# Kernel tuning notes

Hardware: AMD Instinct MI355X
Metric: run time of the kernel (lower is better)

## Reference

```python
import jax, jax.numpy as jnp
import numpy as np

B, L, H, NH = 4, 512, 512, 8
DK = H // NH
REPR_IN, REPR_HID = 53, 32
EPS = 1e-5


def setup_inputs() -> dict:
    key = jax.random.key(0)
    ks = jax.random.split(key, 12)
    x = jax.random.normal(ks[0], (B, L, H), dtype=jnp.float32)
    mask = jax.random.randint(ks[1], (B, L), 0, 2, dtype=jnp.int32)
    refCov = jax.random.normal(ks[2], (B, L, L, REPR_IN), dtype=jnp.float32)
    def lin(k, fan_in, fan_out):
        return jax.random.normal(k, (fan_in, fan_out), dtype=jnp.float32) / np.sqrt(fan_in)
    Wv = lin(ks[3], H, H); bv = jnp.zeros((H,), jnp.float32)
    W1 = lin(ks[4], REPR_IN, REPR_HID); b1 = jnp.zeros((REPR_HID,), jnp.float32)
    W2 = lin(ks[5], REPR_HID, NH); b2 = jnp.zeros((NH,), jnp.float32)
    Wo = lin(ks[6], H, H); bo = jnp.zeros((H,), jnp.float32)
    gamma = jnp.ones((H,), jnp.float32); beta = jnp.zeros((H,), jnp.float32)
    return {"x": x, "mask": mask, "refCov": refCov, "Wv": Wv, "bv": bv,
            "W1": W1, "b1": b1, "W2": W2, "b2": b2, "Wo": Wo, "bo": bo,
            "gamma": gamma, "beta": beta}


def reference(x, mask, refCov, Wv, bv, W1, b1, W2, b2, Wo, bo, gamma, beta):
    Bx, Lx, Hx = x.shape
    residual = x
    # value projection -> (B, NH, L, DK)
    value = (x @ Wv + bv).reshape(Bx, Lx, NH, DK).transpose(0, 2, 1, 3)
    # per-pair MLP on refCov: (B, L, L, 53) -> (B, L, L, NH)
    h1 = jax.nn.relu(refCov @ W1 + b1)
    scores = jnp.transpose(h1 @ W2 + b2, (0, 3, 1, 2))  # (B, NH, L, L)
    # pairwise mask and softmax
    m = mask.astype(bool)
    mask2d = m[:, :, None] & m[:, None, :]              # (B, L, L)
    masked = jnp.where(mask2d[:, None, :, :], scores, -jnp.inf)
    all_inf_rows = ~jnp.any(mask2d, axis=-1)            # (B, L) rows fully masked
    masked = jnp.where(all_inf_rows[:, None, :, None], 0.0, masked)
    attn = jax.nn.softmax(masked, axis=-1)
    # weighted sum and output projection
    out = jnp.einsum('bhij,bhjd->bhid', attn, value)
    out = out.transpose(0, 2, 1, 3).reshape(Bx, Lx, Hx)
    out = out @ Wo + bo
    # residual + LayerNorm
    y = residual + out
    mu = jnp.mean(y, axis=-1, keepdims=True)
    var = jnp.var(y, axis=-1, keepdims=True)
    return (y - mu) / jnp.sqrt(var + EPS) * gamma + beta
```

## Files before the change

kernel.cpp:

```cpp
#include <hip/hip_runtime.h>
#include <hip/hip_bf16.h>
#include <math.h>

#define B 4
#define L 512
#define H 512
#define NH 8
#define DK 64
#define RIN 53
#define RHID 32

using short8 = __attribute__((ext_vector_type(8))) short;
using ushort8v = __attribute__((ext_vector_type(8))) unsigned short;
using f32x4 = __attribute__((ext_vector_type(4))) float;

__device__ __forceinline__ float waveReduceSum(float v) {
#pragma unroll
  for (int off = 32; off > 0; off >>= 1) v += __shfl_xor(v, off, 64);
  return v;
}

__device__ __forceinline__ unsigned short cvt_bf16(float f) {
  __hip_bfloat16 h = __float2bfloat16(f);
  return __builtin_bit_cast(unsigned short, h);
}

__global__ __launch_bounds__(512) void prep_kernel(
    const int* __restrict__ mask, int* __restrict__ jidx, int* __restrict__ nv,
    const float* __restrict__ Wv, const float* __restrict__ Wo,
    unsigned short* __restrict__ WvT, unsigned short* __restrict__ WoT) {
  const int bid = blockIdx.x;
  const int tid = threadIdx.x;
  if (bid < 4) {
    const int b = bid;
    const int lane = tid & 63, wv = tid >> 6;
    __shared__ int wtot[8], woff[8];
    const int m = (mask[b * 512 + tid] != 0);
    const unsigned long long bal = __ballot(m);
    const int lpre = __popcll(bal & ((1ull << lane) - 1ull));
    if (lane == 0) wtot[wv] = __popcll(bal);
    __syncthreads();
    if (tid == 0) {
      int acc = 0;
#pragma unroll
      for (int q = 0; q < 8; ++q) {
        woff[q] = acc;
        acc += wtot[q];
      }
      nv[b] = acc;
    }
    __syncthreads();
    if (m) jidx[b * 512 + woff[wv] + lpre] = tid;
    return;
  }
  const int t = bid - 4;
  const int matsel = t >> 6;
  const int tile = t & 63;
  const float* W = matsel ? Wo : Wv;
  unsigned short* WT = matsel ? WoT : WvT;
  const int k0 = (tile & 7) * 64, n0 = (tile >> 3) * 64;
  __shared__ float sT[64][65];
  {
    const int r = tid >> 3, c0 = (tid & 7) * 8;
    const float4 v0 = *(const float4*)(W + (size_t)(k0 + r) * 512 + n0 + c0);
    const float4 v1 = *(const float4*)(W + (size_t)(k0 + r) * 512 + n0 + c0 + 4);
    sT[r][c0] = v0.x; sT[r][c0 + 1] = v0.y; sT[r][c0 + 2] = v0.z; sT[r][c0 + 3] = v0.w;
    sT[r][c0 + 4] = v1.x; sT[r][c0 + 5] = v1.y; sT[r][c0 + 6] = v1.z; sT[r][c0 + 7] = v1.w;
  }
  __syncthreads();
  {
    const int n = tid >> 3, c0 = (tid & 7) * 8;
    ushort8v o;
#pragma unroll
    for (int cc = 0; cc < 8; ++cc) o[cc] = cvt_bf16(sT[c0 + cc][n]);
    *(ushort8v*)(WT + (size_t)(n0 + n) * 512 + k0 + c0) = o;
  }
}

#define GEMM_SMEM 13824
template <int AMODE, int OMODE>
__device__ __forceinline__ void gemm32x64(
    char* __restrict__ smem, const void* __restrict__ Aq, int lda,
    const unsigned short* __restrict__ Bs, int ldb,
    const float* __restrict__ bias, void* __restrict__ Cp, int ldc) {
  unsigned short* sA = (unsigned short*)smem;
  unsigned short* sB = (unsigned short*)(smem + 4608);
  float(*sC)[68] = (float(*)[68])smem;
  const int tid = threadIdx.x;
  const int w = tid >> 6, l = tid & 63, g = l >> 4, a = l & 15;
  const int wm = (w >> 1) * 16, wn = (w & 1) * 32;
  f32x4 acc0 = {}, acc1 = {};
  const int ar = tid >> 3, ak = (tid & 7) * 8;

  auto loadA = [&](int k0) {
    ushort8v r;
    if constexpr (AMODE == 1) {
      const float* Af = (const float*)Aq;
      const float* p = Af + (size_t)ar * lda + k0 + ak;
      const float4 v0 = *(const float4*)p;
      const float4 v1 = *(const float4*)(p + 4);
      r[0] = cvt_bf16(v0.x); r[1] = cvt_bf16(v0.y);
      r[2] = cvt_bf16(v0.z); r[3] = cvt_bf16(v0.w);
      r[4] = cvt_bf16(v1.x); r[5] = cvt_bf16(v1.y);
      r[6] = cvt_bf16(v1.z); r[7] = cvt_bf16(v1.w);
    } else {
      const unsigned short* Ab = (const unsigned short*)Aq;
      r = *(const ushort8v*)(Ab + (size_t)ar * lda + k0 + ak);
    }
    return r;
  };
  auto loadB = [&](int k0, int q) {
    const int s = tid + q * 256;
    return *(const ushort8v*)(Bs + (size_t)(s >> 3) * ldb + k0 + (s & 7) * 8);
  };

  ushort8v aR = loadA(0);
  ushort8v bR0 = loadB(0, 0), bR1 = loadB(0, 1);
  for (int k0 = 0; k0 < 512; k0 += 64) {
    *(ushort8v*)(&sA[ar * 72 + ak]) = aR;
    *(ushort8v*)(&sB[ar * 72 + ak]) = bR0;
    *(ushort8v*)(&sB[(ar + 32) * 72 + ak]) = bR1;
    __syncthreads();
    if (k0 < 448) {
      aR = loadA(k0 + 64);
      bR0 = loadB(k0 + 64, 0);
      bR1 = loadB(k0 + 64, 1);
    }
#pragma unroll
    for (int ks = 0; ks < 2; ++ks) {
      const short8 af = *(const short8*)(&sA[(wm + a) * 72 + ks * 32 + g * 8]);
      const short8 bf0 = *(const short8*)(&sB[(wn + a) * 72 + ks * 32 + g * 8]);
      const short8 bf1 =
          *(const short8*)(&sB[(wn + 16 + a) * 72 + ks * 32 + g * 8]);
      acc0 = __builtin_amdgcn_mfma_f32_16x16x32_bf16(af, bf0, acc0, 0, 0, 0);
      acc1 = __builtin_amdgcn_mfma_f32_16x16x32_bf16(af, bf1, acc1, 0, 0, 0);
    }
    __syncthreads();
  }

#pragma unroll
  for (int r = 0; r < 4; ++r) {
    sC[wm + g * 4 + r][wn + a] = acc0[r];
    sC[wm + g * 4 + r][wn + 16 + a] = acc1[r];
  }
  __syncthreads();

  if constexpr (OMODE == 2) {
    const int n = tid >> 2, iq = (tid & 3) * 8;
    const float bv = bias ? bias[n] : 0.f;
    ushort8v o;
#pragma unroll
    for (int cc = 0; cc < 8; ++cc) o[cc] = cvt_bf16(sC[iq + cc][n] + bv);
    *(ushort8v*)((unsigned short*)Cp + (size_t)n * ldc + iq) = o;
  } else {
    const int m = tid >> 3, c8 = (tid & 7) * 8;
    float v[8];
#pragma unroll
    for (int cc = 0; cc < 8; ++cc) {
      v[cc] = sC[m][c8 + cc];
      if (bias) v[cc] += bias[c8 + cc];
    }
    if constexpr (OMODE == 1) {
      ushort8v o;
#pragma unroll
      for (int cc = 0; cc < 8; ++cc) o[cc] = cvt_bf16(v[cc]);
      *(ushort8v*)((unsigned short*)Cp + (size_t)m * ldc + c8) = o;
    } else {
      *(float4*)((float*)Cp + (size_t)m * ldc + c8) =
          make_float4(v[0], v[1], v[2], v[3]);
      *(float4*)((float*)Cp + (size_t)m * ldc + c8 + 4) =
          make_float4(v[4], v[5], v[6], v[7]);
    }
  }
}

#define FUSED_SMEM 15616
__global__ __launch_bounds__(256) void fused_scores_value_kernel(
    const float* __restrict__ refCov, const int* __restrict__ mask,
    const int* __restrict__ jidx, const int* __restrict__ nvArr,
    const float* __restrict__ W1, const float* __restrict__ b1,
    const float* __restrict__ W2, const float* __restrict__ b2,
    unsigned short* __restrict__ attnb, const float* __restrict__ x,
    const unsigned short* __restrict__ WvT, const float* __restrict__ bv,
    unsigned short* __restrict__ valT) {
  __shared__ __align__(16) char smem[FUSED_SMEM];
  const int tid = threadIdx.x;

  if (blockIdx.x >= 2048) {
    const int gb = blockIdx.x - 2048;
    const int n0 = (gb & 7) * 64;
    const int m0 = (gb >> 3) * 32;
    const int b = m0 >> 9, i0 = m0 & 511;
    gemm32x64<1, 2>(smem, x + (size_t)m0 * 512, 512, WvT + (size_t)n0 * 512,
                    512, bv + n0,
                    valT + (size_t)b * 262144 + (size_t)n0 * 512 + i0, 512);
    return;
  }

  unsigned short* sH1 = (unsigned short*)smem;
  int* sJ = (int*)(smem + 5120);
  unsigned short* sOut = (unsigned short*)(smem + 7168);
  float(*redbuf)[16] = (float(*)[16])(smem + 15360);

  const int b = blockIdx.x >> 9;
  const int i = blockIdx.x & (L - 1);
  const int w = tid >> 6;
  const int l = tid & 63;
  const int g = l >> 4;
  const int a = l & 15;

  const int mi = mask[b * L + i];
  const int nv = nvArr[b];

  if (mi == 0 || nv == 0) {
    const ushort4 u4 = {0x3B00u, 0x3B00u, 0x3B00u, 0x3B00u};
#pragma unroll
    for (int q = 0; q < 4; ++q) {
      const int f4 = q * 256 + tid;
      const int h = f4 >> 7;
      const int c4 = f4 & 127;
      *(ushort4*)(attnb + ((size_t)(b * NH + h) * L + i) * L + c4 * 4) = u4;
    }
    return;
  }

  sJ[tid] = jidx[b * 512 + tid];
  sJ[tid + 256] = jidx[b * 512 + 256 + tid];

  short8 w1f[2][2];
#pragma unroll
  for (int ks = 0; ks < 2; ++ks)
#pragma unroll
    for (int nt = 0; nt < 2; ++nt)
#pragma unroll
      for (int e = 0; e < 8; ++e) {
        const int k = ks * 32 + g * 8 + e;
        w1f[ks][nt][e] =
            (k < RIN) ? (short)cvt_bf16(W1[k * RHID + nt * 16 + a]) : (short)0;
      }
  short8 w2f;
#pragma unroll
  for (int e = 0; e < 8; ++e) {
    const int k = g * 8 + e;
    w2f[e] = (a < NH) ? (short)cvt_bf16(W2[k * NH + a]) : (short)0;
  }
  const float b1v0 = b1[a];
  const float b1v1 = b1[16 + a];
  const float b2v = (a < NH) ? b2[a] : 0.f;

  __syncthreads();

  const int NT = (nv + 15) >> 4;
  f32x4 sc[8];

#pragma unroll
  for (int mt = 0; mt < 8; ++mt) {
    const int t = mt * 4 + w;
    if (t >= NT) continue;
    const int s = t * 16 + a;
    const int j = sJ[(s < nv) ? s : (nv - 1)];
    const float* rp = refCov + ((size_t)((b << 9) + i) * 512 + j) * RIN;

    const float4 u0 = *(const float4*)(rp + g * 8);
    const float4 u1 = *(const float4*)(rp + g * 8 + 4);
    const int base0 = (g < 3) ? (32 + g * 8) : 32;
    const int base1 = (g == 0) ? 36 : (g == 1) ? 44 : 49;
    const float4 v0 = *(const float4*)(rp + base0);
    const float4 v1 = *(const float4*)(rp + base1);
    float t1[8];
    if (g < 3) {
      t1[0] = v0.x; t1[1] = v0.y; t1[2] = v0.z; t1[3] = v0.w;
    } else {
      t1[0] = 0.f; t1[1] = 0.f; t1[2] = 0.f; t1[3] = 0.f;
    }
    if (g < 2) {
      t1[4] = v1.x; t1[5] = v1.y; t1[6] = v1.z; t1[7] = v1.w;
    } else if (g == 2) {
      t1[4] = v1.w;
      t1[5] = 0.f; t1[6] = 0.f; t1[7] = 0.f;
    } else {
      t1[4] = 0.f; t1[5] = 0.f; t1[6] = 0.f; t1[7] = 0.f;
    }
    short8 af0, af1;
    af0[0] = (short)cvt_bf16(u0.x); af0[1] = (short)cvt_bf16(u0.y);
    af0[2] = (short)cvt_bf16(u0.z); af0[3] = (short)cvt_bf16(u0.w);
    af0[4] = (short)cvt_bf16(u1.x); af0[5] = (short)cvt_bf16(u1.y);
    af0[6] = (short)cvt_bf16(u1.z); af0[7] = (short)cvt_bf16(u1.w);
#pragma unroll
    for (int e = 0; e < 8; ++e) af1[e] = (short)cvt_bf16(t1[e]);

    f32x4 h0 = f32x4{b1v0, b1v0, b1v0, b1v0};
    f32x4 h1v = f32x4{b1v1, b1v1, b1v1, b1v1};
    h0 = __builtin_amdgcn_mfma_f32_16x16x32_bf16(af0, w1f[0][0], h0, 0, 0, 0);
    h1v = __builtin_amdgcn_mfma_f32_16x16x32_bf16(af0, w1f[0][1], h1v, 0, 0, 0);
    h0 = __builtin_amdgcn_mfma_f32_16x16x32_bf16(af1, w1f[1][0], h0, 0, 0, 0);
    h1v = __builtin_amdgcn_mfma_f32_16x16x32_bf16(af1, w1f[1][1], h1v, 0, 0, 0);

#pragma unroll
    for (int r = 0; r < 4; ++r) {
      sH1[(w * 16 + g * 4 + r) * 40 + a] = cvt_bf16(fmaxf(h0[r], 0.f));
      sH1[(w * 16 + g * 4 + r) * 40 + 16 + a] = cvt_bf16(fmaxf(h1v[r], 0.f));
    }

    const short8 af2 = *(const short8*)(&sH1[(w * 16 + a) * 40 + g * 8]);
    f32x4 acc = f32x4{b2v, b2v, b2v, b2v};
    sc[mt] = __builtin_amdgcn_mfma_f32_16x16x32_bf16(af2, w2f, acc, 0, 0, 0);
  }

  float mx = -INFINITY;
#pragma unroll
  for (int mt = 0; mt < 8; ++mt) {
    const int t = mt * 4 + w;
    if (t >= NT) continue;
#pragma unroll
    for (int r = 0; r < 4; ++r) {
      const int s = t * 16 + g * 4 + r;
      if (s < nv) mx = fmaxf(mx, sc[mt][r]);
    }
  }
  mx = fmaxf(mx, __shfl_xor(mx, 16, 64));
  mx = fmaxf(mx, __shfl_xor(mx, 32, 64));
  if (g == 0) redbuf[w][a] = mx;
  __syncthreads();
  const float rmax = fmaxf(fmaxf(redbuf[0][a], redbuf[1][a]),
                           fmaxf(redbuf[2][a], redbuf[3][a]));
  __syncthreads();

  float lsum = 0.f;
#pragma unroll
  for (int mt = 0; mt < 8; ++mt) {
    const int t = mt * 4 + w;
    if (t >= NT) continue;
#pragma unroll
    for (int r = 0; r < 4; ++r) {
      const int s = t * 16 + g * 4 + r;
      const float e = (s < nv) ? __expf(sc[mt][r] - rmax) : 0.f;
      sc[mt][r] = e;
      lsum += e;
    }
  }
  lsum += __shfl_xor(lsum, 16, 64);
  lsum += __shfl_xor(lsum, 32, 64);
  if (g == 0) redbuf[w][a] = lsum;
  __syncthreads();
  const float rsum = redbuf[0][a] + redbuf[1][a] + redbuf[2][a] + redbuf[3][a];
  const float inv = 1.f / rsum;

  {
    const ushort8v z{};
    *(ushort8v*)(&sOut[tid * 16]) = z;
    *(ushort8v*)(&sOut[tid * 16 + 8]) = z;
  }
  __syncthreads();
  if (a < NH) {
#pragma unroll
    for (int mt = 0; mt < 8; ++mt) {
      const int t = mt * 4 + w;
      if (t >= NT) continue;
#pragma unroll
      for (int r = 0; r < 4; ++r) {
        const int s = t * 16 + g * 4 + r;
        if (s < nv) sOut[a * 512 + sJ[s]] = cvt_bf16(sc[mt][r] * inv);
      }
    }
  }
  __syncthreads();
  {
    const int h = tid >> 5, off = (tid & 31) * 16;
    unsigned short* dst = attnb + ((size_t)(b * NH + h) * L + i) * L + off;
    *(ushort8v*)dst = *(const ushort8v*)(&sOut[h * 512 + off]);
    *(ushort8v*)(dst + 8) = *(const ushort8v*)(&sOut[h * 512 + off + 8]);
  }
}

__global__ __launch_bounds__(256) void attn_value_kernel(
    const unsigned short* __restrict__ attnb,
    const unsigned short* __restrict__ valT, unsigned short* __restrict__ ctx) {
  __shared__ __align__(16) char smem[GEMM_SMEM];
  const int bid = blockIdx.x;
  const int it = bid & 15, h = (bid >> 4) & 7, b = bid >> 7;
  const int i0 = it * 32;
  gemm32x64<0, 1>(smem, attnb + ((size_t)((b * 8 + h) * 512 + i0)) * 512, 512,
                  valT + (size_t)b * 262144 + (size_t)(h * 64) * 512, 512,
                  nullptr, ctx + ((size_t)(b * 512 + i0)) * 512 + h * 64, 512);
}

__global__ __launch_bounds__(256) void gemm_proj_kernel(
    const unsigned short* __restrict__ ctx,
    const unsigned short* __restrict__ WoT, const float* __restrict__ bo,
    float* __restrict__ proj) {
  __shared__ __align__(16) char smem[GEMM_SMEM];
  const int n0 = blockIdx.x * 64;
  const int m0 = blockIdx.y * 32;
  gemm32x64<0, 0>(smem, ctx + (size_t)m0 * 512, 512, WoT + (size_t)n0 * 512,
                  512, bo + n0, proj + (size_t)m0 * 512 + n0, 512);
}

__global__ __launch_bounds__(256) void residual_ln_kernel(
    const float* __restrict__ x, const float* __restrict__ proj,
    const float* __restrict__ gamma, const float* __restrict__ beta,
    float* __restrict__ out) {
  const int row = blockIdx.x;
  const int tid = threadIdx.x;
  __shared__ float redS[4], redQ[4];
  float y[2];
  float ls = 0.f, lq = 0.f;
#pragma unroll
  for (int p = 0; p < 2; ++p) {
    const int c = tid + p * 256;
    const float v = x[(size_t)row * H + c] + proj[(size_t)row * H + c];
    y[p] = v;
    ls += v;
    lq += v * v;
  }
  const int lane = tid & 63, wave = tid >> 6;
  ls = waveReduceSum(ls);
  lq = waveReduceSum(lq);
  if (lane == 0) {
    redS[wave] = ls;
    redQ[wave] = lq;
  }
  __syncthreads();
  const float sum = redS[0] + redS[1] + redS[2] + redS[3];
  const float sq = redQ[0] + redQ[1] + redQ[2] + redQ[3];
  const float mu = sum * (1.f / H);
  const float var = sq * (1.f / H) - mu * mu;
  const float inv = rsqrtf(var + 1e-5f);
#pragma unroll
  for (int p = 0; p < 2; ++p) {
    const int c = tid + p * 256;
    out[(size_t)row * H + c] = (y[p] - mu) * inv * gamma[c] + beta[c];
  }
}

extern "C" void kernel_launch(void* const* d_in, const int* in_sizes, int n_in,
                              void* d_out, int out_size, void* d_ws,
                              size_t ws_size, hipStream_t stream) {
  const float* x = (const float*)d_in[0];
  const int* mask = (const int*)d_in[1];
  const float* refCov = (const float*)d_in[2];
  const float* Wv = (const float*)d_in[3];
  const float* bv = (const float*)d_in[4];
  const float* W1 = (const float*)d_in[5];
  const float* b1 = (const float*)d_in[6];
  const float* W2 = (const float*)d_in[7];
  const float* b2 = (const float*)d_in[8];
  const float* Wo = (const float*)d_in[9];
  const float* bo = (const float*)d_in[10];
  const float* gamma = (const float*)d_in[11];
  const float* beta = (const float*)d_in[12];
  float* out = (float*)d_out;

  const size_t n_attn = (size_t)B * NH * L * L;
  const size_t n_blh = (size_t)B * L * H;
  const size_t n_w = (size_t)H * H;
  unsigned short* attnb = (unsigned short*)d_ws;
  unsigned short* valT = attnb + n_attn;
  unsigned short* ctx = valT + n_blh;
  unsigned short* WvT = ctx + n_blh;
  unsigned short* WoT = WvT + n_w;
  float* proj = (float*)(WoT + n_w);
  int* jidx = (int*)(proj + n_blh);
  int* nv = jidx + B * L;
  const size_t needed =
      (n_attn + 2 * n_blh + 2 * n_w) * 2 + n_blh * 4 + (B * L + B) * 4;
  if (ws_size < needed) return;

  const int M = B * L;

  prep_kernel<<<132, 512, 0, stream>>>(mask, jidx, nv, Wv, Wo, WvT, WoT);
  fused_scores_value_kernel<<<2048 + 512, 256, 0, stream>>>(
      refCov, mask, jidx, nv, W1, b1, W2, b2, attnb, x, WvT, bv, valT);
  attn_value_kernel<<<512, 256, 0, stream>>>(attnb, valT, ctx);
  gemm_proj_kernel<<<dim3(8, M / 32), 256, 0, stream>>>(ctx, WoT, bo, proj);
  residual_ln_kernel<<<M, 256, 0, stream>>>(x, proj, gamma, beta, out);
}
```

Before: 61.06 us.

## Fuse output projection GEMM with residual add and LayerNorm

```diff
diff --git a/kernel.cpp b/kernel.cpp
--- a/kernel.cpp
+++ b/kernel.cpp
@@ -13,12 +13,6 @@
 using short8 = __attribute__((ext_vector_type(8))) short;
 using ushort8v = __attribute__((ext_vector_type(8))) unsigned short;
 using f32x4 = __attribute__((ext_vector_type(4))) float;
-
-__device__ __forceinline__ float waveReduceSum(float v) {
-#pragma unroll
-  for (int off = 32; off > 0; off >>= 1) v += __shfl_xor(v, off, 64);
-  return v;
-}
 
 __device__ __forceinline__ unsigned short cvt_bf16(float f) {
   __hip_bfloat16 h = __float2bfloat16(f);
@@ -385,51 +379,101 @@
                   nullptr, ctx + ((size_t)(b * 512 + i0)) * 512 + h * 64, 512);
 }
 
-__global__ __launch_bounds__(256) void gemm_proj_kernel(
+__global__ __launch_bounds__(512) void proj_ln_kernel(
     const unsigned short* __restrict__ ctx,
     const unsigned short* __restrict__ WoT, const float* __restrict__ bo,
-    float* __restrict__ proj) {
-  __shared__ __align__(16) char smem[GEMM_SMEM];
-  const int n0 = blockIdx.x * 64;
-  const int m0 = blockIdx.y * 32;
-  gemm32x64<0, 0>(smem, ctx + (size_t)m0 * 512, 512, WoT + (size_t)n0 * 512,
-                  512, bo + n0, proj + (size_t)m0 * 512 + n0, 512);
-}
-
-__global__ __launch_bounds__(256) void residual_ln_kernel(
-    const float* __restrict__ x, const float* __restrict__ proj,
-    const float* __restrict__ gamma, const float* __restrict__ beta,
-    float* __restrict__ out) {
-  const int row = blockIdx.x;
+    const float* __restrict__ x, const float* __restrict__ gamma,
+    const float* __restrict__ beta, float* __restrict__ out) {
+  __shared__ unsigned short sA[16 * 520];
+  __shared__ float sRs[16][8], sRq[16][8];
   const int tid = threadIdx.x;
-  __shared__ float redS[4], redQ[4];
-  float y[2];
-  float ls = 0.f, lq = 0.f;
-#pragma unroll
-  for (int p = 0; p < 2; ++p) {
-    const int c = tid + p * 256;
-    const float v = x[(size_t)row * H + c] + proj[(size_t)row * H + c];
-    y[p] = v;
-    ls += v;
-    lq += v * v;
-  }
-  const int lane = tid & 63, wave = tid >> 6;
-  ls = waveReduceSum(ls);
-  lq = waveReduceSum(lq);
-  if (lane == 0) {
-    redS[wave] = ls;
-    redQ[wave] = lq;
-  }
-  __syncthreads();
-  const float sum = redS[0] + redS[1] + redS[2] + redS[3];
-  const float sq = redQ[0] + redQ[1] + redQ[2] + redQ[3];
-  const float mu = sum * (1.f / H);
-  const float var = sq * (1.f / H) - mu * mu;
-  const float inv = rsqrtf(var + 1e-5f);
-#pragma unroll
-  for (int p = 0; p < 2; ++p) {
-    const int c = tid + p * 256;
-    out[(size_t)row * H + c] = (y[p] - mu) * inv * gamma[c] + beta[c];
+  const int w = tid >> 6, l = tid & 63, g = l >> 4, a = l & 15;
+  const int m0 = blockIdx.x * 16;
+
+#pragma unroll
+  for (int q = 0; q < 2; ++q) {
+    const int s = tid + q * 512;
+    const int r = s >> 6, c8 = s & 63;
+    *(ushort8v*)(&sA[r * 520 + c8 * 8]) =
+        *(const ushort8v*)(ctx + (size_t)(m0 + r) * 512 + c8 * 8);
+  }
+  __syncthreads();
+
+  const int nbase = w * 64;
+  f32x4 acc[4];
+#pragma unroll
+  for (int ntp = 0; ntp < 2; ++ntp) {
+    const int n0 = nbase + ntp * 32;
+    f32x4 a0 = {}, a1 = {};
+#pragma unroll
+    for (int kc = 0; kc < 16; ++kc) {
+      const short8 af = *(const short8*)(&sA[a * 520 + kc * 32 + g * 8]);
+      const short8 bf0 =
+          *(const short8*)(WoT + (size_t)(n0 + a) * 512 + kc * 32 + g * 8);
+      const short8 bf1 =
+          *(const short8*)(WoT + (size_t)(n0 + 16 + a) * 512 + kc * 32 + g * 8);
+      a0 = __builtin_amdgcn_mfma_f32_16x16x32_bf16(af, bf0, a0, 0, 0, 0);
+      a1 = __builtin_amdgcn_mfma_f32_16x16x32_bf16(af, bf1, a1, 0, 0, 0);
+    }
+    acc[ntp * 2] = a0;
+    acc[ntp * 2 + 1] = a1;
+  }
+
+  float yv[4][4];
+  float sr[4] = {}, qr[4] = {};
+#pragma unroll
+  for (int nt = 0; nt < 4; ++nt) {
+    const int col = nbase + nt * 16 + a;
+    const float bv = bo[col];
+#pragma unroll
+    for (int r = 0; r < 4; ++r) {
+      const int row = g * 4 + r;
+      const float y = acc[nt][r] + bv + x[(size_t)(m0 + row) * 512 + col];
+      yv[nt][r] = y;
+      sr[r] += y;
+      qr[r] += y * y;
+    }
+  }
+#pragma unroll
+  for (int off = 1; off <= 8; off <<= 1)
+#pragma unroll
+    for (int r = 0; r < 4; ++r) {
+      sr[r] += __shfl_xor(sr[r], off, 64);
+      qr[r] += __shfl_xor(qr[r], off, 64);
+    }
+  if (a == 0) {
+#pragma unroll
+    for (int r = 0; r < 4; ++r) {
+      sRs[g * 4 + r][w] = sr[r];
+      sRq[g * 4 + r][w] = qr[r];
+    }
+  }
+  __syncthreads();
+  float mu[4], inv[4];
+#pragma unroll
+  for (int r = 0; r < 4; ++r) {
+    const int row = g * 4 + r;
+    float s = 0.f, q = 0.f;
+#pragma unroll
+    for (int ww = 0; ww < 8; ++ww) {
+      s += sRs[row][ww];
+      q += sRq[row][ww];
+    }
+    mu[r] = s * (1.f / 512.f);
+    const float var = q * (1.f / 512.f) - mu[r] * mu[r];
+    inv[r] = rsqrtf(var + 1e-5f);
+  }
+
+#pragma unroll
+  for (int nt = 0; nt < 4; ++nt) {
+    const int col = nbase + nt * 16 + a;
+    const float gm = gamma[col], bt = beta[col];
+#pragma unroll
+    for (int r = 0; r < 4; ++r) {
+      const int row = g * 4 + r;
+      out[(size_t)(m0 + row) * 512 + col] =
+          (yv[nt][r] - mu[r]) * inv[r] * gm + bt;
+    }
   }
 }
 
@@ -459,19 +503,14 @@
   unsigned short* ctx = valT + n_blh;
   unsigned short* WvT = ctx + n_blh;
   unsigned short* WoT = WvT + n_w;
-  float* proj = (float*)(WoT + n_w);
-  int* jidx = (int*)(proj + n_blh);
+  int* jidx = (int*)(WoT + n_w);
   int* nv = jidx + B * L;
-  const size_t needed =
-      (n_attn + 2 * n_blh + 2 * n_w) * 2 + n_blh * 4 + (B * L + B) * 4;
+  const size_t needed = (n_attn + 2 * n_blh + 2 * n_w) * 2 + (B * L + B) * 4;
   if (ws_size < needed) return;
-
-  const int M = B * L;
 
   prep_kernel<<<132, 512, 0, stream>>>(mask, jidx, nv, Wv, Wo, WvT, WoT);
   fused_scores_value_kernel<<<2048 + 512, 256, 0, stream>>>(
       refCov, mask, jidx, nv, W1, b1, W2, b2, attnb, x, WvT, bv, valT);
   attn_value_kernel<<<512, 256, 0, stream>>>(attnb, valT, ctx);
-  gemm_proj_kernel<<<dim3(8, M / 32), 256, 0, stream>>>(ctx, WoT, bo, proj);
-  residual_ln_kernel<<<M, 256, 0, stream>>>(x, proj, gamma, beta, out);
-}
+  proj_ln_kernel<<<128, 512, 0, stream>>>(ctx, WoT, bo, x, gamma, beta, out);
+}
```

Result: slower. 68.50 us (+12.2%).
